# Kernel tuning notes

Measured on AMD Instinct MI355X. Metric: run time of the kernel, lower is better.

Reference implementation:

```python
import jax, jax.numpy as jnp
import numpy as np

MAX_K = 10
BUF = 50  # buffer_size
HIDDEN = 512


def setup_inputs() -> dict:
    key = jax.random.key(0)
    k1, k2, k3 = jax.random.split(key, 3)
    x = jax.random.normal(k1, (16, 4096, 8), dtype=jnp.float32)
    W = jax.random.normal(k2, (HIDDEN, 1), dtype=jnp.float32) * 0.5  # Linear(1, hidden) weight
    b = jax.random.normal(k3, (HIDDEN,), dtype=jnp.float32) * 0.5    # Linear bias
    return {"x": x, "W": W, "b": b}


def _higuchi_fd(windows):
    # windows: [P, BUF] rolling buffers; vectorized Higuchi fractal dimension.
    n = BUF
    lk_list = []
    for k in range(1, MAX_K + 1):
        acc = jnp.zeros(windows.shape[0], dtype=windows.dtype)
        for m in range(k):
            idxs = np.arange(m, n, k)
            if len(idxs) >= 2:
                seg = windows[:, idxs]  # [P, len(idxs)] static gather
                lengths = jnp.sum(jnp.abs(seg[:, 1:] - seg[:, :-1]), axis=1)
                acc = acc + lengths * ((n - 1) / (len(idxs) * k))
        lk_list.append(acc / k)
    lk = jnp.stack(lk_list, axis=-1)  # [P, MAX_K]
    valid = lk > 0
    w = valid.astype(lk.dtype)
    log_k = jnp.log(jnp.arange(1, MAX_K + 1, dtype=lk.dtype))  # [MAX_K]
    log_lk = jnp.where(valid, jnp.log(jnp.maximum(lk, 1e-30)), 0.0)
    # masked degree-1 least squares: slope of log_lk vs log_k
    Sw = jnp.sum(w, -1)
    Sx = jnp.sum(w * log_k, -1)
    Sy = jnp.sum(w * log_lk, -1)
    Sxx = jnp.sum(w * log_k * log_k, -1)
    Sxy = jnp.sum(w * log_k * log_lk, -1)
    denom = Sw * Sxx - Sx * Sx
    safe = jnp.abs(denom) > 1e-12
    slope = jnp.where(safe, (Sw * Sxy - Sx * Sy) / jnp.where(safe, denom, 1.0), 0.0)
    return jnp.where(Sw > 1, -slope, 0.0)  # [P]


def reference(x, W, b):
    B, S, _ = x.shape
    close = x[:, :, 3].reshape(-1)  # [P] flattened batch-major, matching the rolling buffer order
    P = B * S
    # buffer initialized to zeros: left-pad with BUF-1 zeros, take sliding windows of BUF
    padded = jnp.concatenate([jnp.zeros(BUF - 1, close.dtype), close])
    idx = jnp.arange(P)[:, None] + jnp.arange(BUF)[None, :]  # [P, BUF]
    windows = padded[idx]
    hfd = _higuchi_fd(windows).reshape(B, S)
    tmask = (jnp.arange(S) >= MAX_K).astype(hfd.dtype)  # hfd left at 0 for t < max_k
    h = (hfd * tmask[None, :])[..., None]  # [B, S, 1]
    # Linear(1, hidden): out = h @ W.T + b, then ReLU
    return jax.nn.relu(h * W[:, 0] + b)  # [B, S, HIDDEN]
```

## Files before the change

### kernel.cpp

```cpp
#include <hip/hip_runtime.h>

#define BUF    50
#define MAXK   10
#define NPAD   49
#define BLK    256
#define HIDDEN 512
#define SEQ    4096

__global__ __launch_bounds__(BLK) void fd_kernel(const float* __restrict__ x,
                                                 float* __restrict__ hfd,
                                                 int P) {
    __shared__ float sm[BLK + NPAD];
    const int base = blockIdx.x * BLK;
    for (int j = threadIdx.x; j < BLK + NPAD; j += BLK) {
        const int src = base - NPAD + j;
        sm[j] = (src >= 0 && src < P) ? x[src * 8 + 3] : 0.0f;
    }
    __syncthreads();

    const int p = base + threadIdx.x;
    if (p >= P) return;

    float w[BUF];
#pragma unroll
    for (int j = 0; j < BUF; ++j) w[j] = sm[threadIdx.x + j];

    const float logk_tab[MAXK] = {0.0f,        0.69314718f, 1.09861229f,
                                  1.38629436f, 1.60943791f, 1.79175947f,
                                  1.94591015f, 2.07944154f, 2.19722458f,
                                  2.30258509f};

    float Sw = 0.0f, Sx = 0.0f, Sy = 0.0f, Sxx = 0.0f, Sxy = 0.0f;
#pragma unroll
    for (int k = 1; k <= MAXK; ++k) {
        float acc = 0.0f;
#pragma unroll
        for (int m = 0; m < k; ++m) {
            const int Nm = (NPAD - m) / k + 1;
            if (Nm >= 2) {
                float len = 0.0f;
#pragma unroll
                for (int i = 1; i < Nm; ++i) {
                    len += fabsf(w[m + i * k] - w[m + (i - 1) * k]);
                }
                acc += len * ((float)NPAD / ((float)Nm * (float)k));
            }
        }
        const float lk = acc / (float)k;
        if (lk > 0.0f) {
            const float lg = logk_tab[k - 1];
            const float ly = logf(fmaxf(lk, 1e-30f));
            Sw += 1.0f;
            Sx += lg;
            Sy += ly;
            Sxx += lg * lg;
            Sxy += lg * ly;
        }
    }
    const float denom = Sw * Sxx - Sx * Sx;
    const float slope =
        (fabsf(denom) > 1e-12f) ? (Sw * Sxy - Sx * Sy) / denom : 0.0f;
    float fd = (Sw > 1.0f) ? -slope : 0.0f;

    const int s = p & (SEQ - 1);
    if (s < MAXK) fd = 0.0f;
    hfd[p] = fd;
}

__global__ __launch_bounds__(256) void expand_kernel(
    const float* __restrict__ hfd, const float* __restrict__ W,
    const float* __restrict__ b, float4* __restrict__ out, int total4) {
    const int gid = blockIdx.x * blockDim.x + threadIdx.x;
    if (gid >= total4) return;
    const int p  = gid >> 7;
    const int h4 = gid & 127;
    const float h = hfd[p];
    const float4 Wv = reinterpret_cast<const float4*>(W)[h4];
    const float4 bv = reinterpret_cast<const float4*>(b)[h4];
    float4 o;
    o.x = fmaxf(fmaf(h, Wv.x, bv.x), 0.0f);
    o.y = fmaxf(fmaf(h, Wv.y, bv.y), 0.0f);
    o.z = fmaxf(fmaf(h, Wv.z, bv.z), 0.0f);
    o.w = fmaxf(fmaf(h, Wv.w, bv.w), 0.0f);
    out[gid] = o;
}

extern "C" void kernel_launch(void* const* d_in, const int* in_sizes, int n_in,
                              void* d_out, int out_size, void* d_ws,
                              size_t ws_size, hipStream_t stream) {
    const float* x = (const float*)d_in[0];
    const float* W = (const float*)d_in[1];
    const float* b = (const float*)d_in[2];
    float* out = (float*)d_out;

    const int P = in_sizes[0] / 8;
    float* hfd = (float*)d_ws;

    fd_kernel<<<(P + BLK - 1) / BLK, BLK, 0, stream>>>(x, hfd, P);

    const int total4 = P * (HIDDEN / 4);
    expand_kernel<<<(total4 + 255) / 256, 256, 0, stream>>>(
        hfd, W, b, (float4*)out, total4);
}
```

Measured before the change: 31.95 us.

## Fuse fractal-dimension computation and hidden expansion into one kernel

Merges the FD kernel and the expand kernel into a single launch. Each 256-thread block handles 32 positions: 32 threads compute the Higuchi FD into shared memory, then all threads write the 512-wide ReLU outputs with nontemporal stores. This removes the second launch and the intermediate hfd round trip through global memory. In exchange, only 32 of 256 threads do the serial FD math, so the expansion stalls behind that phase. The grid also assumes P is a multiple of 32.

```diff
diff --git a/kernel.cpp b/kernel.cpp
--- a/kernel.cpp
+++ b/kernel.cpp
@@ -1,104 +1,104 @@
 #include <hip/hip_runtime.h>
 
-#define BUF    50
-#define MAXK   10
-#define NPAD   49
-#define BLK    256
-#define HIDDEN 512
-#define SEQ    4096
+#define BUF     50
+#define MAXK    10
+#define NPAD    49
+#define BLK     256
+#define HIDDEN  512
+#define H4      128
+#define SEQ     4096
+#define PPB     32
 
-__global__ __launch_bounds__(BLK) void fd_kernel(const float* __restrict__ x,
-                                                 float* __restrict__ hfd,
-                                                 int P) {
-    __shared__ float sm[BLK + NPAD];
-    const int base = blockIdx.x * BLK;
-    for (int j = threadIdx.x; j < BLK + NPAD; j += BLK) {
-        const int src = base - NPAD + j;
-        sm[j] = (src >= 0 && src < P) ? x[src * 8 + 3] : 0.0f;
+typedef float v4f __attribute__((ext_vector_type(4)));
+
+__global__ __launch_bounds__(BLK) void fused_kernel(
+    const float* __restrict__ x, const v4f* __restrict__ W4,
+    const v4f* __restrict__ b4, v4f* __restrict__ out, int P) {
+    __shared__ float sm_close[PPB + NPAD];
+    __shared__ float sm_fd[PPB];
+
+    const int base = blockIdx.x * PPB;
+    const int tid = threadIdx.x;
+
+    if (tid < PPB + NPAD) {
+        const int src = base - NPAD + tid;
+        sm_close[tid] = (src >= 0) ? x[src * 8 + 3] : 0.0f;
     }
     __syncthreads();
 
-    const int p = base + threadIdx.x;
-    if (p >= P) return;
+    if (tid < PPB) {
+        float w[BUF];
+#pragma unroll
+        for (int j = 0; j < BUF; ++j) w[j] = sm_close[tid + j];
 
-    float w[BUF];
+        const float logk_tab[MAXK] = {0.0f,        0.69314718f, 1.09861229f,
+                                      1.38629436f, 1.60943791f, 1.79175947f,
+                                      1.94591015f, 2.07944154f, 2.19722458f,
+                                      2.30258509f};
+
+        float Sw = 0.0f, Sx = 0.0f, Sy = 0.0f, Sxx = 0.0f, Sxy = 0.0f;
 #pragma unroll
-    for (int j = 0; j < BUF; ++j) w[j] = sm[threadIdx.x + j];
-
-    const float logk_tab[MAXK] = {0.0f,        0.69314718f, 1.09861229f,
-                                  1.38629436f, 1.60943791f, 1.79175947f,
-                                  1.94591015f, 2.07944154f, 2.19722458f,
-                                  2.30258509f};
-
-    float Sw = 0.0f, Sx = 0.0f, Sy = 0.0f, Sxx = 0.0f, Sxy = 0.0f;
+        for (int k = 1; k <= MAXK; ++k) {
+            float acc = 0.0f;
 #pragma unroll
-    for (int k = 1; k <= MAXK; ++k) {
-        float acc = 0.0f;
+            for (int m = 0; m < k; ++m) {
+                const int Nm = (NPAD - m) / k + 1;
+                if (Nm >= 2) {
+                    float len = 0.0f;
 #pragma unroll
-        for (int m = 0; m < k; ++m) {
-            const int Nm = (NPAD - m) / k + 1;
-            if (Nm >= 2) {
-                float len = 0.0f;
-#pragma unroll
-                for (int i = 1; i < Nm; ++i) {
-                    len += fabsf(w[m + i * k] - w[m + (i - 1) * k]);
+                    for (int i = 1; i < Nm; ++i)
+                        len += fabsf(w[m + i * k] - w[m + (i - 1) * k]);
+                    acc += len * ((float)NPAD / ((float)Nm * (float)k));
                 }
-                acc += len * ((float)NPAD / ((float)Nm * (float)k));
+            }
+            const float lk = acc / (float)k;
+            if (lk > 0.0f) {
+                const float lg = logk_tab[k - 1];
+                const float ly = logf(fmaxf(lk, 1e-30f));
+                Sw += 1.0f;
+                Sx += lg;
+                Sy += ly;
+                Sxx += lg * lg;
+                Sxy += lg * ly;
             }
         }
-        const float lk = acc / (float)k;
-        if (lk > 0.0f) {
-            const float lg = logk_tab[k - 1];
-            const float ly = logf(fmaxf(lk, 1e-30f));
-            Sw += 1.0f;
-            Sx += lg;
-            Sy += ly;
-            Sxx += lg * lg;
-            Sxy += lg * ly;
-        }
+        const float denom = Sw * Sxx - Sx * Sx;
+        const float slope =
+            (fabsf(denom) > 1e-12f) ? (Sw * Sxy - Sx * Sy) / denom : 0.0f;
+        float fd = (Sw > 1.0f) ? -slope : 0.0f;
+
+        const int s = (base + tid) & (SEQ - 1);
+        if (s < MAXK) fd = 0.0f;
+        sm_fd[tid] = fd;
     }
-    const float denom = Sw * Sxx - Sx * Sx;
-    const float slope =
-        (fabsf(denom) > 1e-12f) ? (Sw * Sxy - Sx * Sy) / denom : 0.0f;
-    float fd = (Sw > 1.0f) ? -slope : 0.0f;
+    __syncthreads();
 
-    const int s = p & (SEQ - 1);
-    if (s < MAXK) fd = 0.0f;
-    hfd[p] = fd;
-}
-
-__global__ __launch_bounds__(256) void expand_kernel(
-    const float* __restrict__ hfd, const float* __restrict__ W,
-    const float* __restrict__ b, float4* __restrict__ out, int total4) {
-    const int gid = blockIdx.x * blockDim.x + threadIdx.x;
-    if (gid >= total4) return;
-    const int p  = gid >> 7;
-    const int h4 = gid & 127;
-    const float h = hfd[p];
-    const float4 Wv = reinterpret_cast<const float4*>(W)[h4];
-    const float4 bv = reinterpret_cast<const float4*>(b)[h4];
-    float4 o;
-    o.x = fmaxf(fmaf(h, Wv.x, bv.x), 0.0f);
-    o.y = fmaxf(fmaf(h, Wv.y, bv.y), 0.0f);
-    o.z = fmaxf(fmaf(h, Wv.z, bv.z), 0.0f);
-    o.w = fmaxf(fmaf(h, Wv.w, bv.w), 0.0f);
-    out[gid] = o;
+    const int h4 = tid & (H4 - 1);
+    const int rbase = tid >> 7;
+    const v4f Wv = W4[h4];
+    const v4f bv = b4[h4];
+    v4f* outb = out + (size_t)base * H4 + h4;
+#pragma unroll
+    for (int i = 0; i < PPB / 2; ++i) {
+        const int row = i * 2 + rbase;
+        const float h = sm_fd[row];
+        v4f o;
+        o.x = fmaxf(fmaf(h, Wv.x, bv.x), 0.0f);
+        o.y = fmaxf(fmaf(h, Wv.y, bv.y), 0.0f);
+        o.z = fmaxf(fmaf(h, Wv.z, bv.z), 0.0f);
+        o.w = fmaxf(fmaf(h, Wv.w, bv.w), 0.0f);
+        __builtin_nontemporal_store(o, outb + (size_t)row * H4);
+    }
 }
 
 extern "C" void kernel_launch(void* const* d_in, const int* in_sizes, int n_in,
                               void* d_out, int out_size, void* d_ws,
                               size_t ws_size, hipStream_t stream) {
     const float* x = (const float*)d_in[0];
-    const float* W = (const float*)d_in[1];
-    const float* b = (const float*)d_in[2];
-    float* out = (float*)d_out;
+    const v4f* W4 = (const v4f*)d_in[1];
+    const v4f* b4 = (const v4f*)d_in[2];
+    v4f* out = (v4f*)d_out;
 
     const int P = in_sizes[0] / 8;
-    float* hfd = (float*)d_ws;
-
-    fd_kernel<<<(P + BLK - 1) / BLK, BLK, 0, stream>>>(x, hfd, P);
-
-    const int total4 = P * (HIDDEN / 4);
-    expand_kernel<<<(total4 + 255) / 256, 256, 0, stream>>>(
-        hfd, W, b, (float4*)out, total4);
+    fused_kernel<<<P / PPB, BLK, 0, stream>>>(x, W4, b4, out, P);
 }
```

Result: slower. 33.89 us (+6.1%).
